# Performance work log

Hardware: AMD Instinct MI355X
Metric: run time of the kernel (lower is better)

Reference implementation:

```python
import jax, jax.numpy as jnp
import numpy as np

B, L, D, H = 2, 4096, 1024, 8
DK = D // H   # per-head key dim = 128
DV = D // H   # per-head value dim = 128
K_CONV = 4
CHUNK = 64
EPS = 1e-6


def _rmsnorm(x, w):
    return x * jax.lax.rsqrt(jnp.mean(x * x, axis=-1, keepdims=True) + EPS) * w


def _l2norm(x):
    return x * jax.lax.rsqrt(jnp.sum(x * x, axis=-1, keepdims=True) + EPS)


def _short_conv(x, w):
    # causal depthwise conv (FLA ShortConvolution) + silu. x: [B,L,C], w: [C,K]
    Kc = w.shape[-1]
    Ln = x.shape[1]
    xp = jnp.pad(x, ((0, 0), (Kc - 1, 0), (0, 0)))
    y = xp[:, 0:Ln, :] * w[:, 0]
    for i in range(1, Kc):
        y = y + xp[:, i:i + Ln, :] * w[:, i]
    return jax.nn.silu(y)


def _delta_chunkwise(q, k, v, beta, chunk=CHUNK):
    # q,k: [B,H,L,DK], v: [B,H,L,DV], beta: [B,H,L]
    Bb, Hh, Ll, Dk = q.shape
    Dv = v.shape[-1]
    q = q * (Dk ** -0.5)
    nC = Ll // chunk  # L divisible by chunk here, no padding needed
    qc = q.reshape(Bb, Hh, nC, chunk, Dk).transpose(2, 0, 1, 3, 4)
    kc = k.reshape(Bb, Hh, nC, chunk, Dk).transpose(2, 0, 1, 3, 4)
    vc = v.reshape(Bb, Hh, nC, chunk, Dv).transpose(2, 0, 1, 3, 4)
    bc = beta.reshape(Bb, Hh, nC, chunk).transpose(2, 0, 1, 3)
    eye = jnp.eye(chunk, dtype=q.dtype)
    causal = jnp.tril(jnp.ones((chunk, chunk), dtype=q.dtype))

    def step(S, inp):
        q_c, k_c, v_c, b_c = inp
        kk = jnp.einsum('bhik,bhjk->bhij', k_c, k_c)
        A = eye + jnp.tril(b_c[..., :, None] * kk, k=-1)
        A_inv = jax.lax.linalg.triangular_solve(
            A, jnp.broadcast_to(eye, A.shape), left_side=True, lower=True,
            transpose_a=False, conjugate_a=False, unit_diagonal=False)
        w_ = jnp.einsum('bhij,bhjk->bhik', A_inv, k_c * b_c[..., None])
        u_ = jnp.einsum('bhij,bhjv->bhiv', A_inv, v_c * b_c[..., None])
        v_new = u_ - jnp.einsum('bhik,bhkv->bhiv', w_, S)
        qk = jnp.einsum('bhik,bhjk->bhij', q_c, k_c)
        o = jnp.einsum('bhik,bhkv->bhiv', q_c, S) + jnp.einsum('bhij,bhjv->bhiv', qk * causal, v_new)
        S_new = S + jnp.einsum('bhik,bhiv->bhkv', k_c, v_new)
        return S_new, o

    S0 = jnp.zeros((Bb, Hh, Dk, Dv), dtype=q.dtype)
    S_f, outs = jax.lax.scan(step, S0, (qc, kc, vc, bc))
    out = outs.transpose(1, 2, 0, 3, 4).reshape(Bb, Hh, Ll, Dv)
    return out, S_f


def setup_inputs() -> dict:
    key = jax.random.key(0)
    ks = jax.random.split(key, 9)
    s = 0.02
    return {
        'x': jax.random.normal(ks[0], (B, L, D), jnp.float32),
        'norm_w': jnp.ones((D,), jnp.float32),
        'Wq': jax.random.normal(ks[1], (D, D), jnp.float32) * s,
        'Wk': jax.random.normal(ks[2], (D, D), jnp.float32) * s,
        'Wv': jax.random.normal(ks[3], (D, D), jnp.float32) * s,
        'Wb': jax.random.normal(ks[4], (D, H), jnp.float32) * s,
        'conv_q': jax.random.normal(ks[5], (D, K_CONV), jnp.float32) * 0.3,
        'conv_k': jax.random.normal(ks[6], (D, K_CONV), jnp.float32) * 0.3,
        'conv_v': jax.random.normal(ks[7], (D, K_CONV), jnp.float32) * 0.3,
        'o_norm_w': jnp.ones((DV,), jnp.float32),
        'Wo': jax.random.normal(ks[8], (D, D), jnp.float32) * s,
    }


def reference(x, norm_w, Wq, Wk, Wv, Wb, conv_q, conv_k, conv_v, o_norm_w, Wo):
    h = _rmsnorm(x, norm_w)
    q = _short_conv(h @ Wq, conv_q)
    k = _short_conv(h @ Wk, conv_k)
    v = _short_conv(h @ Wv, conv_v)
    beta = jax.nn.sigmoid(h @ Wb)                      # [B,L,H]
    qh = q.reshape(B, L, H, DK).transpose(0, 2, 1, 3)  # [B,H,L,DK]
    kh = k.reshape(B, L, H, DK).transpose(0, 2, 1, 3)
    vh = v.reshape(B, L, H, DV).transpose(0, 2, 1, 3)
    qh = _l2norm(jax.nn.silu(qh))  # qk_activation=silu, qk_norm=l2
    kh = _l2norm(jax.nn.silu(kh))
    bh = beta.transpose(0, 2, 1)   # [B,H,L]
    o, _ = _delta_chunkwise(qh, kh, vh, bh)
    o = o.transpose(0, 2, 1, 3)    # [B,L,H,DV]
    o = _rmsnorm(o, o_norm_w)      # per-head output RMSNorm
    return x + o.reshape(B, L, D) @ Wo
```

## Files before the change

kernel.cpp:

```cpp
#include <hip/hip_runtime.h>
#include <hip/hip_bf16.h>

#define B_ 2
#define L_ 4096
#define D_ 1024
#define H_ 8
#define DK_ 128
#define NR_ (B_*L_)
#define NC_ 64
#define CS_ 64

typedef __attribute__((ext_vector_type(8))) short short8;
typedef __attribute__((ext_vector_type(4))) float f32x4;

__device__ __forceinline__ float sigmf(float x){ return 1.0f/(1.0f+__expf(-x)); }
__device__ __forceinline__ float siluf(float x){ return x/(1.0f+__expf(-x)); }
__device__ __forceinline__ unsigned short f2bf(float f){
  __hip_bfloat16 h = __float2bfloat16(f);
  return *reinterpret_cast<unsigned short*>(&h);
}
__device__ __forceinline__ void gll16(const void* g, void* l){
  __builtin_amdgcn_global_load_lds((const __attribute__((address_space(1))) void*)g,
      (__attribute__((address_space(3))) void*)l, 16, 0, 0);
}

__global__ __launch_bounds__(256) void rmsnorm_kernel(const float* __restrict__ x,
    const float* __restrict__ w, float* __restrict__ h, unsigned short* __restrict__ hb){
  int n = blockIdx.x; int t = threadIdx.x;
  float4 v = ((const float4*)(x + (size_t)n*D_))[t];
  float ss = v.x*v.x + v.y*v.y + v.z*v.z + v.w*v.w;
  #pragma unroll
  for (int m=32;m>0;m>>=1) ss += __shfl_xor(ss, m, 64);
  __shared__ float red[4];
  if ((t&63)==0) red[t>>6] = ss;
  __syncthreads();
  ss = red[0]+red[1]+red[2]+red[3];
  float rs = rsqrtf(ss*(1.0f/D_) + 1e-6f);
  float4 wv = ((const float4*)w)[t];
  float4 o; o.x=v.x*rs*wv.x; o.y=v.y*rs*wv.y; o.z=v.z*rs*wv.z; o.w=v.w*rs*wv.w;
  ((float4*)(h + (size_t)n*D_))[t] = o;
  ushort4 ob4; ob4.x=f2bf(o.x); ob4.y=f2bf(o.y); ob4.z=f2bf(o.z); ob4.w=f2bf(o.w);
  ((ushort4*)(hb + (size_t)n*D_))[t] = ob4;
}

__global__ __launch_bounds__(256) void transpose_bf16_kernel(const float* __restrict__ W,
    unsigned short* __restrict__ Wt){
  __shared__ float tile[64][65];
  int bi = blockIdx.y, bj = blockIdx.x;
  int tx = threadIdx.x & 63, tg = threadIdx.x >> 6;
  #pragma unroll
  for (int i=0;i<16;i++){
    int r = tg*16 + i;
    tile[r][tx] = W[(size_t)(bi*64 + r)*D_ + bj*64 + tx];
  }
  __syncthreads();
  #pragma unroll
  for (int i=0;i<16;i++){
    int r = tg*16 + i;
    Wt[(size_t)(bj*64 + r)*D_ + bi*64 + tx] = f2bf(tile[tx][r]);
  }
}

__global__ __launch_bounds__(256) void gemm_bf16(const unsigned short* __restrict__ A,
    const unsigned short* __restrict__ Bt, const float* __restrict__ R,
    float* __restrict__ C, int N, int K){
  __shared__ __align__(16) unsigned short Al[4096];
  __shared__ __align__(16) unsigned short Bl[4096];
  int t = threadIdx.x, w = t>>6, l = t&63;
  int wm = w&1, wn = w>>1;
  int row0 = blockIdx.y*128, col0 = blockIdx.x*128;
  int lr = l&15, lk = l>>4;
  const unsigned short* ga0 = A  + (size_t)(row0 + w*16     + lr)*K + lk*8;
  const unsigned short* ga1 = A  + (size_t)(row0 + (w+4)*16 + lr)*K + lk*8;
  const unsigned short* gb0 = Bt + (size_t)(col0 + w*16     + lr)*K + lk*8;
  const unsigned short* gb1 = Bt + (size_t)(col0 + (w+4)*16 + lr)*K + lk*8;
  unsigned short* la0 = &Al[(w*64 + l)*8];
  unsigned short* la1 = &Al[((w+4)*64 + l)*8];
  unsigned short* lb0 = &Bl[(w*64 + l)*8];
  unsigned short* lb1 = &Bl[((w+4)*64 + l)*8];
  f32x4 acc[4][4];
  #pragma unroll
  for (int i=0;i<4;i++)
    #pragma unroll
    for (int j=0;j<4;j++) acc[i][j] = (f32x4){0.f,0.f,0.f,0.f};
  for (int k0=0;k0<K;k0+=32){
    gll16(ga0 + k0, la0);
    gll16(ga1 + k0, la1);
    gll16(gb0 + k0, lb0);
    gll16(gb1 + k0, lb1);
    __syncthreads();
    short8 af[4], bfr[4];
    #pragma unroll
    for (int i=0;i<4;i++) af[i]  = *(const short8*)&Al[((wm*4+i)*64 + l)*8];
    #pragma unroll
    for (int j=0;j<4;j++) bfr[j] = *(const short8*)&Bl[((wn*4+j)*64 + l)*8];
    #pragma unroll
    for (int i=0;i<4;i++)
      #pragma unroll
      for (int j=0;j<4;j++)
        acc[i][j] = __builtin_amdgcn_mfma_f32_16x16x32_bf16(af[i], bfr[j], acc[i][j], 0,0,0);
    __syncthreads();
  }
  int orow = row0 + wm*64 + (l>>4)*4;
  int ocol = col0 + wn*64 + (l&15);
  #pragma unroll
  for (int i=0;i<4;i++){
    #pragma unroll
    for (int j=0;j<4;j++){
      #pragma unroll
      for (int r=0;r<4;r++){
        size_t idx = (size_t)(orow + i*16 + r)*N + ocol + j*16;
        float res = R ? R[idx] : 0.0f;
        C[idx] = acc[i][j][r] + res;
      }
    }
  }
}

__global__ __launch_bounds__(256) void beta_kernel(const float* __restrict__ h,
    const float* __restrict__ Wb, float* __restrict__ beta){
  int n = blockIdx.x, t = threadIdx.x;
  const float* hr = h + (size_t)n*D_;
  float p[8] = {};
  for (int kx=t; kx<D_; kx+=256){
    float hv = hr[kx];
    const float* wr = Wb + (size_t)kx*H_;
    #pragma unroll
    for (int j=0;j<8;j++) p[j] += hv*wr[j];
  }
  #pragma unroll
  for (int m=32;m>0;m>>=1){
    #pragma unroll
    for (int j=0;j<8;j++) p[j] += __shfl_xor(p[j], m, 64);
  }
  __shared__ float red[4][8];
  if ((t&63)==0){
    #pragma unroll
    for (int j=0;j<8;j++) red[t>>6][j] = p[j];
  }
  __syncthreads();
  if (t < 8){
    float s = red[0][t]+red[1][t]+red[2][t]+red[3][t];
    beta[(size_t)n*H_ + t] = sigmf(s);
  }
}

__global__ __launch_bounds__(256) void conv_silu_kernel(const float* __restrict__ in,
    const float* __restrict__ w, float* __restrict__ out){
  size_t idx = (size_t)blockIdx.x*256 + threadIdx.x;
  int c = (int)(idx & (D_-1));
  int n = (int)(idx >> 10);
  int l = n & (L_-1);
  float4 wv = ((const float4*)w)[c];
  float acc = wv.w * in[idx];
  if (l >= 1) acc += wv.z * in[idx - D_];
  if (l >= 2) acc += wv.y * in[idx - 2*D_];
  if (l >= 3) acc += wv.x * in[idx - 3*D_];
  out[idx] = siluf(acc);
}

__global__ __launch_bounds__(256) void silu_l2norm_kernel(float* __restrict__ a, float scale,
    unsigned short* __restrict__ ob){
  int n = blockIdx.x, t = threadIdx.x;
  float* row = a + (size_t)n*D_;
  float4 v = ((const float4*)row)[t];
  float4 u; u.x=siluf(v.x); u.y=siluf(v.y); u.z=siluf(v.z); u.w=siluf(v.w);
  float ss = u.x*u.x+u.y*u.y+u.z*u.z+u.w*u.w;
  #pragma unroll
  for (int m=16;m>0;m>>=1) ss += __shfl_xor(ss, m, 64);
  float rs = rsqrtf(ss + 1e-6f) * scale;
  u.x*=rs; u.y*=rs; u.z*=rs; u.w*=rs;
  ((float4*)row)[t] = u;
  if (ob){
    ushort4 r4; r4.x=f2bf(u.x); r4.y=f2bf(u.y); r4.z=f2bf(u.z); r4.w=f2bf(u.w);
    ((ushort4*)(ob + (size_t)n*D_))[t] = r4;
  }
}

__global__ __launch_bounds__(256) void chunk_local_kernel(
    const float* __restrict__ q, const float* __restrict__ k, const float* __restrict__ v,
    const float* __restrict__ beta, unsigned short* __restrict__ wneg_buf,
    float* __restrict__ u_buf, unsigned short* __restrict__ qk_buf,
    unsigned short* __restrict__ kt_buf){
  int ci = blockIdx.x, bh = blockIdx.y;
  int b = bh >> 3, hh = bh & 7;
  int n0 = b*L_ + ci*CS_;
  int cbase = hh*DK_;
  int cid = bh*NC_ + ci;
  __shared__ float Ks[64][132];
  __shared__ float Als[64*68];
  __shared__ float rowW[144];
  __shared__ float rowU[144];
  __shared__ float bs[64];
  int t = threadIdx.x;
  {
    int r = t >> 2, c0 = (t & 3)*32;
    const float* kr = k + (size_t)(n0+r)*D_ + cbase + c0;
    #pragma unroll
    for (int m=0;m<32;m+=4) *(float4*)&Ks[r][c0+m] = *(const float4*)&kr[m];
  }
  if (t < 64) bs[t] = beta[(size_t)(n0+t)*H_ + hh];
  __syncthreads();
  int ti = t >> 4, tj = t & 15;
  {
    float cc[4][4] = {};
    #pragma unroll 2
    for (int d=0; d<128; d+=4){
      float4 ar[4], br[4];
      #pragma unroll
      for (int r2=0;r2<4;r2++) ar[r2] = *(const float4*)&Ks[ti+16*r2][d];
      #pragma unroll
      for (int s2=0;s2<4;s2++) br[s2] = *(const float4*)&Ks[tj+16*s2][d];
      #pragma unroll
      for (int r2=0;r2<4;r2++){
        #pragma unroll
        for (int s2=0;s2<4;s2++){
          cc[r2][s2] += ar[r2].x*br[s2].x + ar[r2].y*br[s2].y
                      + ar[r2].z*br[s2].z + ar[r2].w*br[s2].w;
        }
      }
    }
    #pragma unroll
    for (int r2=0;r2<4;r2++){
      #pragma unroll
      for (int s2=0;s2<4;s2++){
        int i2 = ti + 16*r2, j2 = tj + 16*s2;
        Als[i2*68 + j2] = (j2 < i2) ? bs[i2]*cc[r2][s2] : 0.0f;
      }
    }
  }
  __syncthreads();
  int i = t >> 2, part = t & 3, ds = part*32, dp = part*36;
  float wreg[32], ureg[32];
  {
    float bi = bs[i];
    const float* vr = v + (size_t)(n0+i)*D_ + cbase + ds;
    #pragma unroll
    for (int m=0;m<32;m++) wreg[m] = bi * Ks[i][ds+m];
    #pragma unroll
    for (int m=0;m<32;m+=4){
      float4 vv = *(const float4*)&vr[m];
      ureg[m+0]=bi*vv.x; ureg[m+1]=bi*vv.y; ureg[m+2]=bi*vv.z; ureg[m+3]=bi*vv.w;
    }
  }
  for (int j=0;j<63;j++){
    if (i == j){
      #pragma unroll
      for (int m=0;m<32;m++){ rowW[dp+m]=wreg[m]; rowU[dp+m]=ureg[m]; }
    }
    __syncthreads();
    if (i > j){
      float aj = Als[i*68 + j];
      #pragma unroll
      for (int m=0;m<32;m++){ wreg[m] -= aj*rowW[dp+m]; ureg[m] -= aj*rowU[dp+m]; }
    }
    __syncthreads();
  }
  {
    unsigned short* wd = wneg_buf + (size_t)cid*(64*128) + (size_t)i*128 + ds;
    float* ud = u_buf + (size_t)cid*(64*128) + (size_t)i*128 + ds;
    #pragma unroll
    for (int m=0;m<32;m+=4){
      ushort4 f; f.x=f2bf(-wreg[m]); f.y=f2bf(-wreg[m+1]); f.z=f2bf(-wreg[m+2]); f.w=f2bf(-wreg[m+3]);
      *(ushort4*)&wd[m] = f;
      float4 g; g.x=ureg[m]; g.y=ureg[m+1]; g.z=ureg[m+2]; g.w=ureg[m+3];
      *(float4*)&ud[m] = g;
    }
  }
  __syncthreads();
  {
    const float* qbase = q + (size_t)n0*D_ + cbase;
    float cc[4][4] = {};
    #pragma unroll 2
    for (int d=0; d<128; d+=4){
      float4 ar[4], br[4];
      #pragma unroll
      for (int r2=0;r2<4;r2++) ar[r2] = *(const float4*)&qbase[(size_t)(ti+16*r2)*D_ + d];
      #pragma unroll
      for (int s2=0;s2<4;s2++) br[s2] = *(const float4*)&Ks[tj+16*s2][d];
      #pragma unroll
      for (int r2=0;r2<4;r2++){
        #pragma unroll
        for (int s2=0;s2<4;s2++){
          cc[r2][s2] += ar[r2].x*br[s2].x + ar[r2].y*br[s2].y
                      + ar[r2].z*br[s2].z + ar[r2].w*br[s2].w;
        }
      }
    }
    unsigned short* qkd = qk_buf + (size_t)cid*4096;
    #pragma unroll
    for (int r2=0;r2<4;r2++){
      #pragma unroll
      for (int s2=0;s2<4;s2++){
        int i2 = ti+16*r2, j2 = tj+16*s2;
        qkd[i2*64 + j2] = (j2 <= i2) ? f2bf(cc[r2][s2]) : (unsigned short)0;
      }
    }
  }
  {
    unsigned short* ktd = kt_buf + (size_t)cid*(64*128);
    for (int idx = t; idx < 8192; idx += 256){
      int d = idx >> 6, i2 = idx & 63;
      ktd[idx] = f2bf(Ks[i2][d]);
    }
  }
}

__global__ __launch_bounds__(256) void seq_kernel(
    const unsigned short* __restrict__ wneg_buf, const float* __restrict__ u_buf,
    const unsigned short* __restrict__ kt_buf, const unsigned short* __restrict__ qk_buf,
    const unsigned short* __restrict__ qbh, float* __restrict__ o_buf){
  int bid = blockIdx.x;
  int bh = bid & 15, cg = bid >> 4;
  int b = bh >> 3, hh = bh & 7;
  int cbase = hh*DK_;
  int t = threadIdx.x;
  int wv = t >> 6, l = t & 63, g = l >> 4, lr = l & 15;

  __shared__ __align__(16) unsigned short Wl[8192];
  __shared__ __align__(16) unsigned short Ql[8192];
  __shared__ __align__(16) unsigned short Ktl[8192];
  __shared__ __align__(16) unsigned short qkl[4096];
  __shared__ __align__(16) float  Ul[2048];
  __shared__ __align__(16) unsigned short Stl[32*136];
  __shared__ __align__(16) float  Sf[32*132];
  __shared__ __align__(16) unsigned short vTl[32*72];

  for (int z=t; z<32*132; z+=256) Sf[z] = 0.0f;
  for (int z=t; z<32*136; z+=256) Stl[z] = 0;
  __syncthreads();

  size_t cid0 = (size_t)bh*NC_;
  const unsigned short* wp  = wneg_buf + cid0*8192;
  const unsigned short* ktp = kt_buf  + cid0*8192;
  const unsigned short* qkp = qk_buf  + cid0*4096;
  const float*          up  = u_buf   + cid0*8192;
  const unsigned short* qp  = qbh + (size_t)(b*L_)*D_ + cbase;

  int wq_kq = wv;
  int hv = wv >> 1, lv = wv & 1;

  for (int ci=0; ci<NC_; ++ci){
    #pragma unroll
    for (int r=0;r<4;r++){
      gll16(wp + (size_t)(16*r + lr)*128 + wq_kq*32 + g*8, &Wl[(r*4+wv)*512 + l*8]);
      gll16(qp + (size_t)(16*r + lr)*D_  + wq_kq*32 + g*8, &Ql[(r*4+wv)*512 + l*8]);
      int fn = 2*r + hv;
      gll16(ktp + (size_t)(16*fn + lr)*64 + lv*32 + g*8, &Ktl[(r*4+wv)*512 + l*8]);
    }
    #pragma unroll
    for (int r=0;r<2;r++){
      int fm = 2*r + hv;
      gll16(qkp + (size_t)(16*fm + lr)*64 + lv*32 + g*8, &qkl[(r*4+wv)*512 + l*8]);
      int idx = r*256 + t;
      gll16(up + (size_t)(idx>>3)*128 + cg*32 + (idx&7)*4, &Ul[idx*4]);
    }
    __syncthreads();

    f32x4 accV[2];
    #pragma unroll
    for (int nt=0;nt<2;nt++){
      #pragma unroll
      for (int r=0;r<4;r++) accV[nt][r] = Ul[(16*wv + 4*g + r)*32 + 16*nt + lr];
    }
    #pragma unroll
    for (int kq=0;kq<4;kq++){
      short8 a = *(const short8*)&Wl[(wv*4+kq)*512 + l*8];
      short8 b0 = *(const short8*)&Stl[(0  + lr)*136 + kq*32 + g*8];
      short8 b1 = *(const short8*)&Stl[(16 + lr)*136 + kq*32 + g*8];
      accV[0] = __builtin_amdgcn_mfma_f32_16x16x32_bf16(a, b0, accV[0], 0,0,0);
      accV[1] = __builtin_amdgcn_mfma_f32_16x16x32_bf16(a, b1, accV[1], 0,0,0);
    }
    #pragma unroll
    for (int nt=0;nt<2;nt++){
      #pragma unroll
      for (int r=0;r<4;r++)
        vTl[(16*nt + lr)*72 + 16*wv + 4*g + r] = f2bf(accV[nt][r]);
    }
    __syncthreads();

    f32x4 accO[2];
    accO[0] = (f32x4){0.f,0.f,0.f,0.f}; accO[1] = (f32x4){0.f,0.f,0.f,0.f};
    #pragma unroll
    for (int kq=0;kq<4;kq++){
      short8 a = *(const short8*)&Ql[(wv*4+kq)*512 + l*8];
      short8 b0 = *(const short8*)&Stl[(0  + lr)*136 + kq*32 + g*8];
      short8 b1 = *(const short8*)&Stl[(16 + lr)*136 + kq*32 + g*8];
      accO[0] = __builtin_amdgcn_mfma_f32_16x16x32_bf16(a, b0, accO[0], 0,0,0);
      accO[1] = __builtin_amdgcn_mfma_f32_16x16x32_bf16(a, b1, accO[1], 0,0,0);
    }
    #pragma unroll
    for (int kq=0;kq<2;kq++){
      short8 a = *(const short8*)&qkl[(wv*2+kq)*512 + l*8];
      short8 b0 = *(const short8*)&vTl[(0  + lr)*72 + kq*32 + g*8];
      short8 b1 = *(const short8*)&vTl[(16 + lr)*72 + kq*32 + g*8];
      accO[0] = __builtin_amdgcn_mfma_f32_16x16x32_bf16(a, b0, accO[0], 0,0,0);
      accO[1] = __builtin_amdgcn_mfma_f32_16x16x32_bf16(a, b1, accO[1], 0,0,0);
    }
    {
      int n0 = b*L_ + ci*CS_;
      #pragma unroll
      for (int nt=0;nt<2;nt++){
        #pragma unroll
        for (int r=0;r<4;r++)
          o_buf[(size_t)(n0 + 16*wv + 4*g + r)*D_ + cbase + cg*32 + 16*nt + lr] = accO[nt][r];
      }
    }
    __syncthreads();

    f32x4 accS[2][2];
    #pragma unroll
    for (int mc=0;mc<2;mc++)
      #pragma unroll
      for (int ntl=0;ntl<2;ntl++)
        #pragma unroll
        for (int r=0;r<4;r++)
          accS[mc][ntl][r] = Sf[(16*mc + 4*g + r)*132 + 32*wv + 16*ntl + lr];
    #pragma unroll
    for (int kq=0;kq<2;kq++){
      short8 a0 = *(const short8*)&vTl[(0  + lr)*72 + kq*32 + g*8];
      short8 a1 = *(const short8*)&vTl[(16 + lr)*72 + kq*32 + g*8];
      short8 b0 = *(const short8*)&Ktl[((2*wv+0)*2 + kq)*512 + l*8];
      short8 b1 = *(const short8*)&Ktl[((2*wv+1)*2 + kq)*512 + l*8];
      accS[0][0] = __builtin_amdgcn_mfma_f32_16x16x32_bf16(a0, b0, accS[0][0], 0,0,0);
      accS[0][1] = __builtin_amdgcn_mfma_f32_16x16x32_bf16(a0, b1, accS[0][1], 0,0,0);
      accS[1][0] = __builtin_amdgcn_mfma_f32_16x16x32_bf16(a1, b0, accS[1][0], 0,0,0);
      accS[1][1] = __builtin_amdgcn_mfma_f32_16x16x32_bf16(a1, b1, accS[1][1], 0,0,0);
    }
    #pragma unroll
    for (int mc=0;mc<2;mc++){
      #pragma unroll
      for (int ntl=0;ntl<2;ntl++){
        #pragma unroll
        for (int r=0;r<4;r++){
          int c = 16*mc + 4*g + r, d = 32*wv + 16*ntl + lr;
          float val = accS[mc][ntl][r];
          Sf[c*132 + d] = val;
          Stl[c*136 + d] = f2bf(val);
        }
      }
    }
    __syncthreads();

    wp += 8192; ktp += 8192; qkp += 4096; up += 8192; qp += (size_t)CS_*D_;
  }
}

__global__ __launch_bounds__(256) void head_rmsnorm_kernel(const float* __restrict__ o,
    const float* __restrict__ w, unsigned short* __restrict__ out){
  int n = blockIdx.x, t = threadIdx.x;
  float4 v = ((const float4*)(o + (size_t)n*D_))[t];
  float ss = v.x*v.x+v.y*v.y+v.z*v.z+v.w*v.w;
  #pragma unroll
  for (int m=16;m>0;m>>=1) ss += __shfl_xor(ss, m, 64);
  float rs = rsqrtf(ss*(1.0f/DK_) + 1e-6f);
  float4 wv = ((const float4*)w)[t & 31];
  float4 u; u.x=v.x*rs*wv.x; u.y=v.y*rs*wv.y; u.z=v.z*rs*wv.z; u.w=v.w*rs*wv.w;
  ushort4 r4; r4.x=f2bf(u.x); r4.y=f2bf(u.y); r4.z=f2bf(u.z); r4.w=f2bf(u.w);
  ((ushort4*)(out + (size_t)n*D_))[t] = r4;
}

extern "C" void kernel_launch(void* const* d_in, const int* in_sizes, int n_in,
                              void* d_out, int out_size, void* d_ws, size_t ws_size,
                              hipStream_t stream){
  const float* x      = (const float*)d_in[0];
  const float* norm_w = (const float*)d_in[1];
  const float* Wq     = (const float*)d_in[2];
  const float* Wk     = (const float*)d_in[3];
  const float* Wv     = (const float*)d_in[4];
  const float* Wb     = (const float*)d_in[5];
  const float* conv_q = (const float*)d_in[6];
  const float* conv_k = (const float*)d_in[7];
  const float* conv_v = (const float*)d_in[8];
  const float* onw    = (const float*)d_in[9];
  const float* Wo     = (const float*)d_in[10];
  float* out = (float*)d_out;

  const size_t NB = (size_t)NR_*D_;
  float* ws   = (float*)d_ws;
  float* h    = ws;
  float* b1   = ws + NB;
  float* b2   = ws + 2*NB;
  float* b3   = ws + 3*NB;
  float* qb   = ws + 4*NB;
  float* kb   = ws + 5*NB;
  float* vb   = ws + 6*NB;
  float* qkb_old = ws + 7*NB;
  float* betab= qkb_old + (size_t)1024*4096;
  unsigned short* wtq = (unsigned short*)(betab + 65536);
  unsigned short* wtk = wtq + (size_t)D_*D_;
  unsigned short* wtv = wtk + (size_t)D_*D_;
  unsigned short* wto = wtv + (size_t)D_*D_;
  unsigned short* hb  = (unsigned short*)qb;
  unsigned short* obb = (unsigned short*)h;
  unsigned short* wneg= (unsigned short*)b1;
  unsigned short* ktb = wneg + NB;
  unsigned short* qkbf= (unsigned short*)b3;
  unsigned short* qbh = qkbf + (size_t)1024*4096;

  rmsnorm_kernel<<<NR_, 256, 0, stream>>>(x, norm_w, h, hb);
  dim3 tg(16,16);
  transpose_bf16_kernel<<<tg, 256, 0, stream>>>(Wq, wtq);
  transpose_bf16_kernel<<<tg, 256, 0, stream>>>(Wk, wtk);
  transpose_bf16_kernel<<<tg, 256, 0, stream>>>(Wv, wtv);
  transpose_bf16_kernel<<<tg, 256, 0, stream>>>(Wo, wto);
  dim3 gg(D_/128, NR_/128);
  gemm_bf16<<<gg, 256, 0, stream>>>(hb, wtq, nullptr, b1, D_, D_);
  gemm_bf16<<<gg, 256, 0, stream>>>(hb, wtk, nullptr, b2, D_, D_);
  gemm_bf16<<<gg, 256, 0, stream>>>(hb, wtv, nullptr, b3, D_, D_);
  beta_kernel<<<NR_, 256, 0, stream>>>(h, Wb, betab);
  conv_silu_kernel<<<(int)(NB/256), 256, 0, stream>>>(b1, conv_q, qb);
  conv_silu_kernel<<<(int)(NB/256), 256, 0, stream>>>(b2, conv_k, kb);
  conv_silu_kernel<<<(int)(NB/256), 256, 0, stream>>>(b3, conv_v, vb);
  const float qscale = 0.08838834764831845f;
  silu_l2norm_kernel<<<NR_, 256, 0, stream>>>(qb, qscale, qbh);
  silu_l2norm_kernel<<<NR_, 256, 0, stream>>>(kb, 1.0f, nullptr);
  chunk_local_kernel<<<dim3(NC_, 16), 256, 0, stream>>>(qb, kb, vb, betab,
      wneg, b2, qkbf, ktb);
  seq_kernel<<<64, 256, 0, stream>>>(wneg, b2, ktb, qkbf, qbh, vb);
  head_rmsnorm_kernel<<<NR_, 256, 0, stream>>>(vb, onw, obb);
  gemm_bf16<<<gg, 256, 0, stream>>>(obb, wto, x, out, D_, D_);
  (void)in_sizes; (void)n_in; (void)out_size; (void)ws_size;
}
```

Before: 777.3 us.

## Double-buffer seq_kernel loads, keep state in registers, fuse QKV projection GEMM

The sequential delta-rule kernel now prefetches the next chunk's operands into a second LDS buffer while computing the current chunk. The fp32 state stays in MFMA accumulator registers instead of round-tripping through shared memory, and full __syncthreads are replaced by explicit waitcnt plus barrier. Separately, the three Q/K/V projection GEMMs become one GEMM over a concatenated weight of width 3*D, with the conv kernel reading via a stride argument. This relies on wtq/wtk/wtv being contiguous and on gemm_bf16 handling N=3D with this layout. It also doubles LDS use in seq_kernel.

Result: faster. 744.2 us (-4.3%).

```diff
diff --git a/kernel.cpp b/kernel.cpp
--- a/kernel.cpp
+++ b/kernel.cpp
@@ -146,17 +146,18 @@
 }
 
 __global__ __launch_bounds__(256) void conv_silu_kernel(const float* __restrict__ in,
-    const float* __restrict__ w, float* __restrict__ out){
+    const float* __restrict__ w, float* __restrict__ out, int ld){
   size_t idx = (size_t)blockIdx.x*256 + threadIdx.x;
   int c = (int)(idx & (D_-1));
   int n = (int)(idx >> 10);
   int l = n & (L_-1);
+  const float* src = in + (size_t)n*ld + c;
   float4 wv = ((const float4*)w)[c];
-  float acc = wv.w * in[idx];
-  if (l >= 1) acc += wv.z * in[idx - D_];
-  if (l >= 2) acc += wv.y * in[idx - 2*D_];
-  if (l >= 3) acc += wv.x * in[idx - 3*D_];
-  out[idx] = siluf(acc);
+  float acc = wv.w * src[0];
+  if (l >= 1) acc += wv.z * src[-ld];
+  if (l >= 2) acc += wv.y * src[-2*ld];
+  if (l >= 3) acc += wv.x * src[-3*ld];
+  out[(size_t)n*D_ + c] = siluf(acc);
 }
 
 __global__ __launch_bounds__(256) void silu_l2norm_kernel(float* __restrict__ a, float scale,
@@ -317,55 +318,73 @@
   int t = threadIdx.x;
   int wv = t >> 6, l = t & 63, g = l >> 4, lr = l & 15;
 
-  __shared__ __align__(16) unsigned short Wl[8192];
-  __shared__ __align__(16) unsigned short Ql[8192];
-  __shared__ __align__(16) unsigned short Ktl[8192];
-  __shared__ __align__(16) unsigned short qkl[4096];
-  __shared__ __align__(16) float  Ul[2048];
+  __shared__ __align__(16) unsigned short Wl[2][8192];
+  __shared__ __align__(16) unsigned short Ql[2][8192];
+  __shared__ __align__(16) unsigned short Ktl[2][8192];
+  __shared__ __align__(16) unsigned short qkl[2][4096];
+  __shared__ __align__(16) float  Ul[2][2048];
   __shared__ __align__(16) unsigned short Stl[32*136];
-  __shared__ __align__(16) float  Sf[32*132];
   __shared__ __align__(16) unsigned short vTl[32*72];
 
-  for (int z=t; z<32*132; z+=256) Sf[z] = 0.0f;
+  f32x4 Sacc[2][2];
+  #pragma unroll
+  for (int mc=0;mc<2;mc++)
+    #pragma unroll
+    for (int ntl=0;ntl<2;ntl++) Sacc[mc][ntl] = (f32x4){0.f,0.f,0.f,0.f};
+
   for (int z=t; z<32*136; z+=256) Stl[z] = 0;
   __syncthreads();
 
   size_t cid0 = (size_t)bh*NC_;
-  const unsigned short* wp  = wneg_buf + cid0*8192;
-  const unsigned short* ktp = kt_buf  + cid0*8192;
-  const unsigned short* qkp = qk_buf  + cid0*4096;
-  const float*          up  = u_buf   + cid0*8192;
-  const unsigned short* qp  = qbh + (size_t)(b*L_)*D_ + cbase;
-
-  int wq_kq = wv;
+  const unsigned short* wb_  = wneg_buf + cid0*8192;
+  const unsigned short* ktb_ = kt_buf  + cid0*8192;
+  const unsigned short* qkb_ = qk_buf  + cid0*4096;
+  const float*          ub_  = u_buf   + cid0*8192;
+  const unsigned short* qb_  = qbh + (size_t)(b*L_)*D_ + cbase;
+
   int hv = wv >> 1, lv = wv & 1;
 
+  #define STAGE(BI, CI) do { \
+    const unsigned short* wp  = wb_  + (size_t)(CI)*8192; \
+    const unsigned short* kp  = ktb_ + (size_t)(CI)*8192; \
+    const unsigned short* qkp = qkb_ + (size_t)(CI)*4096; \
+    const float*          up  = ub_  + (size_t)(CI)*8192; \
+    const unsigned short* qp  = qb_  + (size_t)(CI)*CS_*D_; \
+    _Pragma("unroll") \
+    for (int r=0;r<4;r++){ \
+      gll16(wp + (size_t)(16*r + lr)*128 + wv*32 + g*8, &Wl[BI][(r*4+wv)*512 + l*8]); \
+      gll16(qp + (size_t)(16*r + lr)*D_  + wv*32 + g*8, &Ql[BI][(r*4+wv)*512 + l*8]); \
+      int fn = 2*r + hv; \
+      gll16(kp + (size_t)(16*fn + lr)*64 + lv*32 + g*8, &Ktl[BI][(r*4+wv)*512 + l*8]); \
+    } \
+    _Pragma("unroll") \
+    for (int r=0;r<2;r++){ \
+      int fm = 2*r + hv; \
+      gll16(qkp + (size_t)(16*fm + lr)*64 + lv*32 + g*8, &qkl[BI][(r*4+wv)*512 + l*8]); \
+      int idx = r*256 + t; \
+      gll16(up + (size_t)(idx>>3)*128 + cg*32 + (idx&7)*4, &Ul[BI][idx*4]); \
+    } \
+  } while(0)
+
+  STAGE(0, 0);
+  asm volatile("s_waitcnt vmcnt(0)" ::: "memory");
+  __builtin_amdgcn_s_barrier();
+  __builtin_amdgcn_sched_barrier(0);
+
+  int cur = 0;
   for (int ci=0; ci<NC_; ++ci){
-    #pragma unroll
-    for (int r=0;r<4;r++){
-      gll16(wp + (size_t)(16*r + lr)*128 + wq_kq*32 + g*8, &Wl[(r*4+wv)*512 + l*8]);
-      gll16(qp + (size_t)(16*r + lr)*D_  + wq_kq*32 + g*8, &Ql[(r*4+wv)*512 + l*8]);
-      int fn = 2*r + hv;
-      gll16(ktp + (size_t)(16*fn + lr)*64 + lv*32 + g*8, &Ktl[(r*4+wv)*512 + l*8]);
-    }
-    #pragma unroll
-    for (int r=0;r<2;r++){
-      int fm = 2*r + hv;
-      gll16(qkp + (size_t)(16*fm + lr)*64 + lv*32 + g*8, &qkl[(r*4+wv)*512 + l*8]);
-      int idx = r*256 + t;
-      gll16(up + (size_t)(idx>>3)*128 + cg*32 + (idx&7)*4, &Ul[idx*4]);
-    }
-    __syncthreads();
+    int cn = (ci+1 < NC_) ? ci+1 : ci;
+    STAGE(cur^1, cn);
 
     f32x4 accV[2];
     #pragma unroll
     for (int nt=0;nt<2;nt++){
       #pragma unroll
-      for (int r=0;r<4;r++) accV[nt][r] = Ul[(16*wv + 4*g + r)*32 + 16*nt + lr];
+      for (int r=0;r<4;r++) accV[nt][r] = Ul[cur][(16*wv + 4*g + r)*32 + 16*nt + lr];
     }
     #pragma unroll
     for (int kq=0;kq<4;kq++){
-      short8 a = *(const short8*)&Wl[(wv*4+kq)*512 + l*8];
+      short8 a  = *(const short8*)&Wl[cur][(wv*4+kq)*512 + l*8];
       short8 b0 = *(const short8*)&Stl[(0  + lr)*136 + kq*32 + g*8];
       short8 b1 = *(const short8*)&Stl[(16 + lr)*136 + kq*32 + g*8];
       accV[0] = __builtin_amdgcn_mfma_f32_16x16x32_bf16(a, b0, accV[0], 0,0,0);
@@ -377,13 +396,15 @@
       for (int r=0;r<4;r++)
         vTl[(16*nt + lr)*72 + 16*wv + 4*g + r] = f2bf(accV[nt][r]);
     }
-    __syncthreads();
+    asm volatile("s_waitcnt lgkmcnt(0)" ::: "memory");
+    __builtin_amdgcn_s_barrier();
+    __builtin_amdgcn_sched_barrier(0);
 
     f32x4 accO[2];
     accO[0] = (f32x4){0.f,0.f,0.f,0.f}; accO[1] = (f32x4){0.f,0.f,0.f,0.f};
     #pragma unroll
     for (int kq=0;kq<4;kq++){
-      short8 a = *(const short8*)&Ql[(wv*4+kq)*512 + l*8];
+      short8 a  = *(const short8*)&Ql[cur][(wv*4+kq)*512 + l*8];
       short8 b0 = *(const short8*)&Stl[(0  + lr)*136 + kq*32 + g*8];
       short8 b1 = *(const short8*)&Stl[(16 + lr)*136 + kq*32 + g*8];
       accO[0] = __builtin_amdgcn_mfma_f32_16x16x32_bf16(a, b0, accO[0], 0,0,0);
@@ -391,7 +412,7 @@
     }
     #pragma unroll
     for (int kq=0;kq<2;kq++){
-      short8 a = *(const short8*)&qkl[(wv*2+kq)*512 + l*8];
+      short8 a  = *(const short8*)&qkl[cur][(wv*2+kq)*512 + l*8];
       short8 b0 = *(const short8*)&vTl[(0  + lr)*72 + kq*32 + g*8];
       short8 b1 = *(const short8*)&vTl[(16 + lr)*72 + kq*32 + g*8];
       accO[0] = __builtin_amdgcn_mfma_f32_16x16x32_bf16(a, b0, accO[0], 0,0,0);
@@ -406,44 +427,37 @@
           o_buf[(size_t)(n0 + 16*wv + 4*g + r)*D_ + cbase + cg*32 + 16*nt + lr] = accO[nt][r];
       }
     }
-    __syncthreads();
-
-    f32x4 accS[2][2];
-    #pragma unroll
-    for (int mc=0;mc<2;mc++)
-      #pragma unroll
-      for (int ntl=0;ntl<2;ntl++)
-        #pragma unroll
-        for (int r=0;r<4;r++)
-          accS[mc][ntl][r] = Sf[(16*mc + 4*g + r)*132 + 32*wv + 16*ntl + lr];
+    asm volatile("s_waitcnt lgkmcnt(0)" ::: "memory");
+    __builtin_amdgcn_s_barrier();
+    __builtin_amdgcn_sched_barrier(0);
+
     #pragma unroll
     for (int kq=0;kq<2;kq++){
       short8 a0 = *(const short8*)&vTl[(0  + lr)*72 + kq*32 + g*8];
       short8 a1 = *(const short8*)&vTl[(16 + lr)*72 + kq*32 + g*8];
-      short8 b0 = *(const short8*)&Ktl[((2*wv+0)*2 + kq)*512 + l*8];
-      short8 b1 = *(const short8*)&Ktl[((2*wv+1)*2 + kq)*512 + l*8];
-      accS[0][0] = __builtin_amdgcn_mfma_f32_16x16x32_bf16(a0, b0, accS[0][0], 0,0,0);
-      accS[0][1] = __builtin_amdgcn_mfma_f32_16x16x32_bf16(a0, b1, accS[0][1], 0,0,0);
-      accS[1][0] = __builtin_amdgcn_mfma_f32_16x16x32_bf16(a1, b0, accS[1][0], 0,0,0);
-      accS[1][1] = __builtin_amdgcn_mfma_f32_16x16x32_bf16(a1, b1, accS[1][1], 0,0,0);
+      short8 b0 = *(const short8*)&Ktl[cur][((2*wv+0)*2 + kq)*512 + l*8];
+      short8 b1 = *(const short8*)&Ktl[cur][((2*wv+1)*2 + kq)*512 + l*8];
+      Sacc[0][0] = __builtin_amdgcn_mfma_f32_16x16x32_bf16(a0, b0, Sacc[0][0], 0,0,0);
+      Sacc[0][1] = __builtin_amdgcn_mfma_f32_16x16x32_bf16(a0, b1, Sacc[0][1], 0,0,0);
+      Sacc[1][0] = __builtin_amdgcn_mfma_f32_16x16x32_bf16(a1, b0, Sacc[1][0], 0,0,0);
+      Sacc[1][1] = __builtin_amdgcn_mfma_f32_16x16x32_bf16(a1, b1, Sacc[1][1], 0,0,0);
     }
     #pragma unroll
     for (int mc=0;mc<2;mc++){
       #pragma unroll
       for (int ntl=0;ntl<2;ntl++){
         #pragma unroll
-        for (int r=0;r<4;r++){
-          int c = 16*mc + 4*g + r, d = 32*wv + 16*ntl + lr;
-          float val = accS[mc][ntl][r];
-          Sf[c*132 + d] = val;
-          Stl[c*136 + d] = f2bf(val);
-        }
-      }
-    }
-    __syncthreads();
-
-    wp += 8192; ktp += 8192; qkp += 4096; up += 8192; qp += (size_t)CS_*D_;
-  }
+        for (int r=0;r<4;r++)
+          Stl[(16*mc + 4*g + r)*136 + 32*wv + 16*ntl + lr] = f2bf(Sacc[mc][ntl][r]);
+      }
+    }
+    asm volatile("s_waitcnt lgkmcnt(0)" ::: "memory");
+    asm volatile("s_waitcnt vmcnt(4)" ::: "memory");
+    __builtin_amdgcn_s_barrier();
+    __builtin_amdgcn_sched_barrier(0);
+    cur ^= 1;
+  }
+  #undef STAGE
 }
 
 __global__ __launch_bounds__(256) void head_rmsnorm_kernel(const float* __restrict__ o,
@@ -479,24 +493,22 @@
   const size_t NB = (size_t)NR_*D_;
   float* ws   = (float*)d_ws;
   float* h    = ws;
-  float* b1   = ws + NB;
-  float* b2   = ws + 2*NB;
-  float* b3   = ws + 3*NB;
+  float* qkv  = ws + NB;
   float* qb   = ws + 4*NB;
   float* kb   = ws + 5*NB;
   float* vb   = ws + 6*NB;
-  float* qkb_old = ws + 7*NB;
-  float* betab= qkb_old + (size_t)1024*4096;
+  float* betab= ws + 7*NB;
   unsigned short* wtq = (unsigned short*)(betab + 65536);
   unsigned short* wtk = wtq + (size_t)D_*D_;
   unsigned short* wtv = wtk + (size_t)D_*D_;
   unsigned short* wto = wtv + (size_t)D_*D_;
   unsigned short* hb  = (unsigned short*)qb;
   unsigned short* obb = (unsigned short*)h;
-  unsigned short* wneg= (unsigned short*)b1;
-  unsigned short* ktb = wneg + NB;
-  unsigned short* qkbf= (unsigned short*)b3;
-  unsigned short* qbh = qkbf + (size_t)1024*4096;
+  unsigned short* wneg = (unsigned short*)qkv;
+  unsigned short* ktb  = wneg + (size_t)8*1024*1024;
+  unsigned short* qkbf = ktb  + (size_t)8*1024*1024;
+  unsigned short* qbh  = qkbf + (size_t)4*1024*1024;
+  float*          ubuf = (float*)(qbh + (size_t)8*1024*1024);
 
   rmsnorm_kernel<<<NR_, 256, 0, stream>>>(x, norm_w, h, hb);
   dim3 tg(16,16);
@@ -504,21 +516,20 @@
   transpose_bf16_kernel<<<tg, 256, 0, stream>>>(Wk, wtk);
   transpose_bf16_kernel<<<tg, 256, 0, stream>>>(Wv, wtv);
   transpose_bf16_kernel<<<tg, 256, 0, stream>>>(Wo, wto);
-  dim3 gg(D_/128, NR_/128);
-  gemm_bf16<<<gg, 256, 0, stream>>>(hb, wtq, nullptr, b1, D_, D_);
-  gemm_bf16<<<gg, 256, 0, stream>>>(hb, wtk, nullptr, b2, D_, D_);
-  gemm_bf16<<<gg, 256, 0, stream>>>(hb, wtv, nullptr, b3, D_, D_);
+  dim3 gq(3*D_/128, NR_/128);
+  gemm_bf16<<<gq, 256, 0, stream>>>(hb, wtq, nullptr, qkv, 3*D_, D_);
   beta_kernel<<<NR_, 256, 0, stream>>>(h, Wb, betab);
-  conv_silu_kernel<<<(int)(NB/256), 256, 0, stream>>>(b1, conv_q, qb);
-  conv_silu_kernel<<<(int)(NB/256), 256, 0, stream>>>(b2, conv_k, kb);
-  conv_silu_kernel<<<(int)(NB/256), 256, 0, stream>>>(b3, conv_v, vb);
+  conv_silu_kernel<<<(int)(NB/256), 256, 0, stream>>>(qkv,        conv_q, qb, 3*D_);
+  conv_silu_kernel<<<(int)(NB/256), 256, 0, stream>>>(qkv + D_,   conv_k, kb, 3*D_);
+  conv_silu_kernel<<<(int)(NB/256), 256, 0, stream>>>(qkv + 2*D_, conv_v, vb, 3*D_);
   const float qscale = 0.08838834764831845f;
   silu_l2norm_kernel<<<NR_, 256, 0, stream>>>(qb, qscale, qbh);
   silu_l2norm_kernel<<<NR_, 256, 0, stream>>>(kb, 1.0f, nullptr);
   chunk_local_kernel<<<dim3(NC_, 16), 256, 0, stream>>>(qb, kb, vb, betab,
-      wneg, b2, qkbf, ktb);
-  seq_kernel<<<64, 256, 0, stream>>>(wneg, b2, ktb, qkbf, qbh, vb);
+      wneg, ubuf, qkbf, ktb);
+  seq_kernel<<<64, 256, 0, stream>>>(wneg, ubuf, ktb, qkbf, qbh, vb);
   head_rmsnorm_kernel<<<NR_, 256, 0, stream>>>(vb, onw, obb);
+  dim3 gg(D_/128, NR_/128);
   gemm_bf16<<<gg, 256, 0, stream>>>(obb, wto, x, out, D_, D_);
   (void)in_sizes; (void)n_in; (void)out_size; (void)ws_size;
 }
```
